# Kernel tuning notes

Hardware: AMD Instinct MI355X
Metric: run time of the kernel (lower is better)

## Reference

```python
import jax, jax.numpy as jnp
import numpy as np
import math

D_MODEL = 2048
HEAD_DIM = 128
NUM_Q_HEADS = 16
NUM_KV_GROUPS = 4


def setup_inputs() -> dict:
    key = jax.random.key(0)
    ks = jax.random.split(key, 9)
    B, S, D = 2, 2048, D_MODEL
    G, HD = NUM_KV_GROUPS, HEAD_DIM
    sd = 1.0 / math.sqrt(D)
    x = jax.random.normal(ks[0], (B, S, D), dtype=jnp.float32)
    # weights stored as [in, out]
    Wq = jax.random.normal(ks[1], (D, D), dtype=jnp.float32) * sd
    bq = jax.random.normal(ks[2], (D,), dtype=jnp.float32) * sd
    Wk = jax.random.normal(ks[3], (D, G * HD), dtype=jnp.float32) * sd
    bk = jax.random.normal(ks[4], (G * HD,), dtype=jnp.float32) * sd
    Wv = jax.random.normal(ks[5], (D, G * HD), dtype=jnp.float32) * sd
    bv = jax.random.normal(ks[6], (G * HD,), dtype=jnp.float32) * sd
    Wo = jax.random.normal(ks[7], (D, D), dtype=jnp.float32) * sd
    bo = jax.random.normal(ks[8], (D,), dtype=jnp.float32) * sd
    return {"x": x, "Wq": Wq, "bq": bq, "Wk": Wk, "bk": bk,
            "Wv": Wv, "bv": bv, "Wo": Wo, "bo": bo}


def reference(x, Wq, bq, Wk, bk, Wv, bv, Wo, bo):
    B, S, D = x.shape
    H, G, HD = NUM_Q_HEADS, NUM_KV_GROUPS, HEAD_DIM
    R = H // G  # q heads per kv group (repeat_interleave factor)
    scale = 1.0 / math.sqrt(HD)
    # projections
    Q = (x @ Wq + bq).reshape(B, S, G, R, HD)   # heads grouped: head h = g*R + r
    K = (x @ Wk + bk).reshape(B, S, G, HD)
    V = (x @ Wv + bv).reshape(B, S, G, HD)
    # scores [B,G,R,S,S]; avoid materializing repeated K/V
    scores = jnp.einsum('bsgrd,btgd->bgrst', Q, K) * scale
    attn = jax.nn.softmax(scores, axis=-1)
    out = jnp.einsum('bgrst,btgd->bsgrd', attn, V)  # [B,S,G,R,HD]
    out = out.reshape(B, S, H * HD)
    return out @ Wo + bo
```

## Files before the change

kernel.cpp:

```cpp
#include <hip/hip_runtime.h>

#define D_MODEL 2048
#define GHD 512
#define HD 128
#define NQH 16
#define B_SZ 2
#define SEQ 2048
#define M_TOT (B_SZ * SEQ)

typedef _Float16 f16;
typedef __fp16 h16x2 __attribute__((ext_vector_type(2)));
typedef _Float16 f16x4 __attribute__((ext_vector_type(4)));
typedef _Float16 f16x8 __attribute__((ext_vector_type(8)));
typedef float f32x4 __attribute__((ext_vector_type(4)));

typedef const __attribute__((address_space(1))) void gvoid;
typedef __attribute__((address_space(3))) void lvoid;
typedef __attribute__((address_space(3))) f16 lf16;

#define BAR() do { asm volatile("" ::: "memory"); \
                   __builtin_amdgcn_s_barrier();  \
                   asm volatile("" ::: "memory"); } while (0)
#define WAIT_VM8() asm volatile("s_waitcnt vmcnt(8)" ::: "memory")
#define WAIT_VM0() asm volatile("s_waitcnt vmcnt(0)" ::: "memory")
#define WAIT_LGKM(N) do { asm volatile("s_waitcnt lgkmcnt(" #N ")" ::: "memory"); \
                          __builtin_amdgcn_sched_barrier(0); } while (0)

template<int OFF>
__device__ __forceinline__ f16x4 tr16(unsigned a) {
    f16x4 d;
    asm volatile("ds_read_b64_tr_b16 %0, %1 offset:%2"
                 : "=v"(d) : "v"(a), "i"(OFF));
    return d;
}

__global__ __launch_bounds__(256) void cast_f16(
    const float* __restrict__ X, f16* __restrict__ Xh)
{
    const size_t i = ((size_t)blockIdx.x * 256 + threadIdx.x) * 8;
    const float4 v0 = *(const float4*)(X + i);
    const float4 v1 = *(const float4*)(X + i + 4);
    f16x8 h;
    h[0] = (f16)v0.x; h[1] = (f16)v0.y; h[2] = (f16)v0.z; h[3] = (f16)v0.w;
    h[4] = (f16)v1.x; h[5] = (f16)v1.y; h[6] = (f16)v1.z; h[7] = (f16)v1.w;
    *(f16x8*)(Xh + i) = h;
}

__global__ __launch_bounds__(256) void transpose_cast(
    const float* __restrict__ W, f16* __restrict__ Th,
    int K, int N, int row_off)
{
    __shared__ float Ls[32][33];
    const int t = threadIdx.x;
    const int n0 = blockIdx.x << 5, k0 = blockIdx.y << 5;
    {
        const int kr = t >> 3, nq = (t & 7) << 2;
        const float4 v = *(const float4*)&W[(size_t)(k0 + kr) * N + n0 + nq];
        Ls[kr][nq + 0] = v.x; Ls[kr][nq + 1] = v.y;
        Ls[kr][nq + 2] = v.z; Ls[kr][nq + 3] = v.w;
    }
    __syncthreads();
    const int nr = t >> 3, kq = (t & 7) << 2;
    f16x4 hv;
#pragma unroll
    for (int e = 0; e < 4; ++e) hv[e] = (f16)Ls[kq + e][nr];
    *(f16x4*)&Th[(size_t)(row_off + n0 + nr) * K + k0 + kq] = hv;
}

template<int BN, bool OUT32>
__global__ __launch_bounds__(256) void gemm_bk64(
    const f16* __restrict__ Agh,
    const f16* __restrict__ BTh,
    const float* __restrict__ bias0, const float* __restrict__ bias1,
    void* __restrict__ C0v, void* __restrict__ C1v,
    int Nsplit, int ld0, int ld1, int K, float outscale)
{
    constexpr int WN = BN / 64;
    constexpr int WM = 4 / WN;
    constexpr int WI = 128 / (WM * 16);
    constexpr int LDK = 72;
    constexpr int NBP = BN / 32;

    __shared__ f16 Ah[128 * LDK];
    __shared__ f16 Bh[BN * LDK];

    const int tid = threadIdx.x;
    const int l = tid & 63, w = tid >> 6;
    const int l15 = l & 15, lq = l >> 4;
    const int wr = w / WN, wc = w % WN;

    const int nwgx = gridDim.x;
    const int orig = blockIdx.y * nwgx + blockIdx.x;
    const int cpx = (nwgx * gridDim.y) >> 3;
    const int sw = (orig & 7) * cpx + (orig >> 3);
    const int m0 = (sw / nwgx) << 7;
    const int n0 = (sw % nwgx) * BN;

    f32x4 acc[WI][4];
#pragma unroll
    for (int i = 0; i < WI; ++i)
#pragma unroll
        for (int j = 0; j < 4; ++j) acc[i][j] = (f32x4){0.f, 0.f, 0.f, 0.f};

    const int srow = tid >> 3;
    const int skc  = (tid & 7) << 3;
    const f16* Ap = Agh + (size_t)(m0 + srow) * K + skc;
    const f16* Bp = BTh + (size_t)(n0 + srow) * K + skc;

    f16x8 av[4], bv[NBP];
#pragma unroll
    for (int p = 0; p < 4; ++p)
        av[p] = *(const f16x8*)(Ap + (size_t)(p * 32) * K);
#pragma unroll
    for (int p = 0; p < NBP; ++p)
        bv[p] = *(const f16x8*)(Bp + (size_t)(p * 32) * K);

    for (int k0 = 0; k0 < K; k0 += 64) {
        __syncthreads();
#pragma unroll
        for (int p = 0; p < 4; ++p)
            *(f16x8*)&Ah[(srow + p * 32) * LDK + skc] = av[p];
#pragma unroll
        for (int p = 0; p < NBP; ++p)
            *(f16x8*)&Bh[(srow + p * 32) * LDK + skc] = bv[p];
        __syncthreads();

        const int kn = k0 + 64;
#pragma unroll
        for (int p = 0; p < 4; ++p)
            av[p] = *(const f16x8*)(Ap + (size_t)(p * 32) * K + kn);
#pragma unroll
        for (int p = 0; p < NBP; ++p)
            bv[p] = *(const f16x8*)(Bp + (size_t)(p * 32) * K + kn);

#pragma unroll
        for (int c = 0; c < 2; ++c) {
            f16x8 afh[WI];
#pragma unroll
            for (int i = 0; i < WI; ++i) {
                const int row = wr * (WI * 16) + i * 16 + l15;
                afh[i] = *(const f16x8*)&Ah[row * LDK + c * 32 + lq * 8];
            }
#pragma unroll
            for (int j = 0; j < 4; ++j) {
                const int bn = wc * 64 + j * 16 + l15;
                const f16x8 bfh = *(const f16x8*)&Bh[bn * LDK + c * 32 + lq * 8];
#pragma unroll
                for (int i = 0; i < WI; ++i)
                    acc[i][j] = __builtin_amdgcn_mfma_f32_16x16x32_f16(afh[i], bfh, acc[i][j], 0, 0, 0);
            }
        }
    }

#pragma unroll
    for (int j = 0; j < 4; ++j) {
        const int ng = n0 + wc * 64 + j * 16 + l15;
        const bool first = ng < Nsplit;
        const float bvf = first ? bias0[ng] : bias1[ng - Nsplit];
        const int nc = first ? ng : ng - Nsplit;
        const int ldc = first ? ld0 : ld1;
#pragma unroll
        for (int i = 0; i < WI; ++i) {
            const int mg = m0 + wr * (WI * 16) + i * 16 + lq * 4;
#pragma unroll
            for (int r = 0; r < 4; ++r) {
                const float v = (acc[i][j][r] + bvf) * outscale;
                if (OUT32)
                    ((float*)(first ? C0v : C1v))[(size_t)(mg + r) * ldc + nc] = v;
                else
                    ((f16*)(first ? C0v : C1v))[(size_t)(mg + r) * ldc + nc] = (f16)v;
            }
        }
    }
}

#define SHUF8(x, y) __builtin_shufflevector(x, y, 0, 1, 2, 3, 4, 5, 6, 7)

__global__ __launch_bounds__(256, 2) void flash_attn_mfma(
    const f16* __restrict__ Q, const f16* __restrict__ Kp,
    const f16* __restrict__ Vp, f16* __restrict__ AOh)
{
    __shared__ f16 KsA[2][64 * 128];
    __shared__ f16 VtA[2][64 * 128];

    const int tid = threadIdx.x;
    const int w = tid >> 6, l = tid & 63;
    const int l15 = l & 15, lq = l >> 4;
    const int b = blockIdx.z, h = blockIdx.y, g = h >> 2;
    const int q0 = blockIdx.x << 7;

    const f16* Qb = Q + (size_t)(b * SEQ + q0) * D_MODEL + h * HD;
    const f16* Kb = Kp + (size_t)b * SEQ * GHD + g * HD;
    const f16* Vb = Vp + (size_t)b * SEQ * GHD + g * HD;

    f16x8 aq[2][4];
#pragma unroll
    for (int rg = 0; rg < 2; ++rg) {
        const f16* qrow = Qb + (size_t)(w * 32 + rg * 16 + l15) * D_MODEL;
#pragma unroll
        for (int c = 0; c < 4; ++c)
            aq[rg][c] = *(const f16x8*)(qrow + c * 32 + lq * 8);
    }

    lf16* Ks3 = (lf16*)&KsA[0][0];
    lf16* Vt3 = (lf16*)&VtA[0][0];
    const f16* ksrc[4]; lf16* kdst[4];
    const f16* vsrc[4]; lf16* vdst[4];
#pragma unroll
    for (int i = 0; i < 4; ++i) {
        const int s = tid + (i << 8);
        {
            const int row = s >> 4, ul = s & 15;
            ksrc[i] = Kb + (size_t)row * GHD + ((ul ^ (row & 7)) << 3);
            kdst[i] = Ks3 + s * 8;
        }
        {
            const int dbit = s & 1, kvlo = (s >> 1) & 3, vlq = (s >> 3) & 3;
            const int jh = (s >> 5) & 1, kc = (s >> 6) & 1, dsub = s >> 7;
            const int kv = (kc << 5) | (jh << 4) | (vlq << 2) | kvlo;
            vsrc[i] = Vb + (size_t)kv * GHD + ((dsub << 4) | (dbit << 3));
            vdst[i] = Vt3 + s * 8;
        }
    }
    const unsigned vta0 = (unsigned)(size_t)(Vt3 + l * 4);
    const unsigned vta1 = vta0 + 16384;

    f32x4 acc_o[2][8];
#pragma unroll
    for (int rg = 0; rg < 2; ++rg)
#pragma unroll
        for (int i = 0; i < 8; ++i) acc_o[rg][i] = (f32x4){0.f, 0.f, 0.f, 0.f};
    float m_q[2] = {-1e30f, -1e30f};
    float l_q[2] = {0.f, 0.f};

    auto issue_tile = [&](int buf, int tile) {
        const size_t koff = (size_t)tile * 64 * GHD;
        const int KO = buf << 13;
#pragma unroll
        for (int i = 0; i < 4; ++i)
            __builtin_amdgcn_global_load_lds((gvoid*)(ksrc[i] + koff),
                                             (lvoid*)(kdst[i] + KO), 16, 0, 0);
#pragma unroll
        for (int i = 0; i < 4; ++i)
            __builtin_amdgcn_global_load_lds((gvoid*)(vsrc[i] + koff),
                                             (lvoid*)(vdst[i] + KO), 16, 0, 0);
    };

    auto compute_tile = [&](const f16* KsB, unsigned vtaB) {
        f32x4 sa[2][4];
        __builtin_amdgcn_s_setprio(1);
#pragma unroll
        for (int cb = 0; cb < 4; ++cb) {
            sa[0][cb] = (f32x4){0.f, 0.f, 0.f, 0.f};
            sa[1][cb] = (f32x4){0.f, 0.f, 0.f, 0.f};
#pragma unroll
            for (int c = 0; c < 4; ++c) {
                const int rk = cb * 16 + l15;
                const f16x8 bk = *(const f16x8*)&KsB[rk * 128 + (((c * 4 + lq) ^ (rk & 7)) << 3)];
                sa[0][cb] = __builtin_amdgcn_mfma_f32_16x16x32_f16(bk, aq[0][c], sa[0][cb], 0, 0, 0);
                sa[1][cb] = __builtin_amdgcn_mfma_f32_16x16x32_f16(bk, aq[1][c], sa[1][cb], 0, 0, 0);
            }
        }
        __builtin_amdgcn_s_setprio(0);

#pragma unroll
        for (int rg = 0; rg < 2; ++rg) {
            float gm = sa[rg][0][0];
#pragma unroll
            for (int cb = 0; cb < 4; ++cb)
#pragma unroll
                for (int reg = 0; reg < 4; ++reg)
                    gm = fmaxf(gm, sa[rg][cb][reg]);
            gm = fmaxf(gm, __shfl_xor(gm, 16));
            gm = fmaxf(gm, __shfl_xor(gm, 32));
            if (__ballot(gm > m_q[rg] + 11.5f)) {
                const float mnew = fmaxf(m_q[rg], gm);
                const float alpha = __builtin_amdgcn_exp2f(m_q[rg] - mnew);
                m_q[rg] = mnew;
                l_q[rg] *= alpha;
                f32x4 av;
#pragma unroll
                for (int reg = 0; reg < 4; ++reg)
                    av[reg] = __shfl(alpha, lq * 4 + reg);
#pragma unroll
                for (int db = 0; db < 8; ++db) acc_o[rg][db] *= av;
            }
        }

        f16x4 va0 = tr16<0>(vtaB),    vb0 = tr16<512>(vtaB);
        f16x4 va1 = tr16<1024>(vtaB), vb1 = tr16<1536>(vtaB);
        f16x4 ca0 = tr16<2048>(vtaB), cb0 = tr16<2560>(vtaB);
        f16x4 ca1 = tr16<3072>(vtaB), cb1 = tr16<3584>(vtaB);

        f16x8 pa[2][2];
#pragma unroll
        for (int rg = 0; rg < 2; ++rg) {
            float ps = 0.f;
#pragma unroll
            for (int cb = 0; cb < 4; ++cb)
#pragma unroll
                for (int reg = 0; reg < 4; ++reg) {
                    const float p = __builtin_amdgcn_exp2f(sa[rg][cb][reg] - m_q[rg]);
                    sa[rg][cb][reg] = p;
                    ps += p;
                }
            l_q[rg] += ps;
#pragma unroll
            for (int kc = 0; kc < 2; ++kc) {
                union { h16x2 h2[4]; f16x8 h8; } u;
                u.h2[0] = __builtin_amdgcn_cvt_pkrtz(sa[rg][2 * kc][0], sa[rg][2 * kc][1]);
                u.h2[1] = __builtin_amdgcn_cvt_pkrtz(sa[rg][2 * kc][2], sa[rg][2 * kc][3]);
                u.h2[2] = __builtin_amdgcn_cvt_pkrtz(sa[rg][2 * kc + 1][0], sa[rg][2 * kc + 1][1]);
                u.h2[3] = __builtin_amdgcn_cvt_pkrtz(sa[rg][2 * kc + 1][2], sa[rg][2 * kc + 1][3]);
                pa[rg][kc] = u.h8;
            }
        }

        WAIT_LGKM(4);
        f16x8 v0 = SHUF8(va0, vb0), v1 = SHUF8(va1, vb1);
#pragma unroll
        for (int db = 0; db < 8; ++db) {
            f16x4 ma0, mb0, ma1, mb1;
            if (db < 6) {
                switch (db) {
                case 0: ma0=tr16<4096>(vtaB);  mb0=tr16<4608>(vtaB);  ma1=tr16<5120>(vtaB);  mb1=tr16<5632>(vtaB);  break;
                case 1: ma0=tr16<6144>(vtaB);  mb0=tr16<6656>(vtaB);  ma1=tr16<7168>(vtaB);  mb1=tr16<7680>(vtaB);  break;
                case 2: ma0=tr16<8192>(vtaB);  mb0=tr16<8704>(vtaB);  ma1=tr16<9216>(vtaB);  mb1=tr16<9728>(vtaB);  break;
                case 3: ma0=tr16<10240>(vtaB); mb0=tr16<10752>(vtaB); ma1=tr16<11264>(vtaB); mb1=tr16<11776>(vtaB); break;
                case 4: ma0=tr16<12288>(vtaB); mb0=tr16<12800>(vtaB); ma1=tr16<13312>(vtaB); mb1=tr16<13824>(vtaB); break;
                default:ma0=tr16<14336>(vtaB); mb0=tr16<14848>(vtaB); ma1=tr16<15360>(vtaB); mb1=tr16<15872>(vtaB); break;
                }
                WAIT_LGKM(4);
            } else if (db == 6) {
                WAIT_LGKM(0);
            }
            f16x8 n0, n1;
            if (db < 7) { n0 = SHUF8(ca0, cb0); n1 = SHUF8(ca1, cb1); }
            __builtin_amdgcn_s_setprio(1);
            acc_o[0][db] = __builtin_amdgcn_mfma_f32_16x16x32_f16(pa[0][0], v0, acc_o[0][db], 0, 0, 0);
            acc_o[1][db] = __builtin_amdgcn_mfma_f32_16x16x32_f16(pa[1][0], v0, acc_o[1][db], 0, 0, 0);
            acc_o[0][db] = __builtin_amdgcn_mfma_f32_16x16x32_f16(pa[0][1], v1, acc_o[0][db], 0, 0, 0);
            acc_o[1][db] = __builtin_amdgcn_mfma_f32_16x16x32_f16(pa[1][1], v1, acc_o[1][db], 0, 0, 0);
            __builtin_amdgcn_s_setprio(0);
            if (db < 7) {
                v0 = n0; v1 = n1;
                ca0 = ma0; cb0 = mb0; ca1 = ma1; cb1 = mb1;
            }
        }
    };

    issue_tile(0, 0);
#pragma unroll 1
    for (int t2 = 0; t2 < 16; ++t2) {
        const int kt0 = t2 << 1;
        issue_tile(1, kt0 + 1);
        WAIT_VM8();
        BAR();
        compute_tile(&KsA[0][0], vta0);
        BAR();
        if (t2 < 15) {
            issue_tile(0, kt0 + 2);
            WAIT_VM8();
        } else {
            WAIT_VM0();
        }
        BAR();
        compute_tile(&KsA[1][0], vta1);
        BAR();
    }

    const size_t obase = (size_t)(b * SEQ + q0 + w * 32) * D_MODEL + h * HD;
#pragma unroll
    for (int rg = 0; rg < 2; ++rg) {
        float lr = l_q[rg];
        lr += __shfl_xor(lr, 16);
        lr += __shfl_xor(lr, 32);
        float inv_l[4];
#pragma unroll
        for (int reg = 0; reg < 4; ++reg)
            inv_l[reg] = 1.f / __shfl(lr, lq * 4 + reg);
#pragma unroll
        for (int db = 0; db < 8; ++db) {
#pragma unroll
            for (int reg = 0; reg < 4; ++reg) {
                const size_t off = obase + (size_t)(rg * 16 + lq * 4 + reg) * D_MODEL + db * 16 + l15;
                AOh[off] = (f16)(acc_o[rg][db][reg] * inv_l[reg]);
            }
        }
    }
}

extern "C" void kernel_launch(void* const* d_in, const int* in_sizes, int n_in,
                              void* d_out, int out_size, void* d_ws, size_t ws_size,
                              hipStream_t stream)
{
    const float* x  = (const float*)d_in[0];
    const float* Wq = (const float*)d_in[1];
    const float* bq = (const float*)d_in[2];
    const float* Wk = (const float*)d_in[3];
    const float* bk = (const float*)d_in[4];
    const float* Wv = (const float*)d_in[5];
    const float* bv = (const float*)d_in[6];
    const float* Wo = (const float*)d_in[7];
    const float* bo = (const float*)d_in[8];
    float* out = (float*)d_out;

    f16* base  = (f16*)d_ws;
    f16* xh    = base;
    f16* WkvT  = base + 16777216;
    f16* WqoT  = base + 20971520;
    f16* Qp    = base + 29360128;
    f16* Kp    = base + 37748736;
    f16* Vp    = base + 39845888;
    f16* AOh   = xh;

    const dim3 blk(256);
    const float qscale = 0.08838834764831845f * 1.4426950408889634f;

    cast_f16<<<dim3(M_TOT * D_MODEL / 8 / 256), blk, 0, stream>>>(x, xh);
    transpose_cast<<<dim3(64, 64), blk, 0, stream>>>(Wq, WqoT, 2048, 2048, 0);
    transpose_cast<<<dim3(16, 64), blk, 0, stream>>>(Wk, WkvT, 2048, 512, 0);
    transpose_cast<<<dim3(16, 64), blk, 0, stream>>>(Wv, WkvT, 2048, 512, 512);

    gemm_bk64<128, false><<<dim3(16, 32), blk, 0, stream>>>(
        xh, WqoT, bq, bq, Qp, Qp, 2048, 2048, 2048, 2048, qscale);
    gemm_bk64<64, false><<<dim3(16, 32), blk, 0, stream>>>(
        xh, WkvT, bk, bv, Kp, Vp, 512, 512, 512, 2048, 1.0f);

    transpose_cast<<<dim3(64, 64), blk, 0, stream>>>(Wo, WqoT, 2048, 2048, 0);

    flash_attn_mfma<<<dim3(SEQ / 128, NQH, B_SZ), blk, 0, stream>>>(Qp, Kp, Vp, AOh);

    gemm_bk64<128, true><<<dim3(16, 32), blk, 0, stream>>>(
        AOh, WqoT, bo, bo, out, out, 2048, 2048, 2048, 2048, 1.0f);
}
```

Measured before the change: 227.4 us.

## Fuse Q/K/V projections into one GEMM and use BK=128 for output projection

Concatenates transposed Wq, Wk and Wv into one weight buffer and runs a single GEMM with a 24x32 grid that routes each column block to Q, K or V with the matching bias and scale. This removes a kernel launch and the low-occupancy separate KV GEMM. The GEMM is also templated on BK, and the output projection now uses BK=128, which halves its K-loop iterations at the cost of more shared memory and registers per block. The workspace layout is compacted to match.

Result: slower. 238.4 us (+4.9%).

```diff
diff --git a/kernel.cpp b/kernel.cpp
--- a/kernel.cpp
+++ b/kernel.cpp
@@ -67,19 +67,24 @@
     *(f16x4*)&Th[(size_t)(row_off + n0 + nr) * K + k0 + kq] = hv;
 }
 
-template<int BN, bool OUT32>
-__global__ __launch_bounds__(256) void gemm_bk64(
-    const f16* __restrict__ Agh,
-    const f16* __restrict__ BTh,
-    const float* __restrict__ bias0, const float* __restrict__ bias1,
-    void* __restrict__ C0v, void* __restrict__ C1v,
-    int Nsplit, int ld0, int ld1, int K, float outscale)
+template<int BN, int BK, bool QKV>
+__global__ __launch_bounds__(256) void gemm_f16(
+    const f16* __restrict__ Agh, const f16* __restrict__ BTh,
+    const float* __restrict__ b0, const float* __restrict__ b1,
+    const float* __restrict__ b2,
+    f16* __restrict__ Qo, f16* __restrict__ Ko, f16* __restrict__ Vo,
+    float* __restrict__ Fo,
+    int K, float qscale)
 {
     constexpr int WN = BN / 64;
     constexpr int WM = 4 / WN;
     constexpr int WI = 128 / (WM * 16);
-    constexpr int LDK = 72;
-    constexpr int NBP = BN / 32;
+    constexpr int LDK = BK + 8;
+    constexpr int CH  = BK / 8;
+    constexpr int RPP = 256 / CH;
+    constexpr int AP  = 128 / RPP;
+    constexpr int BP  = BN / RPP;
+    constexpr int NC  = BK / 32;
 
     __shared__ f16 Ah[128 * LDK];
     __shared__ f16 Bh[BN * LDK];
@@ -102,39 +107,39 @@
 #pragma unroll
         for (int j = 0; j < 4; ++j) acc[i][j] = (f32x4){0.f, 0.f, 0.f, 0.f};
 
-    const int srow = tid >> 3;
-    const int skc  = (tid & 7) << 3;
+    const int srow = tid / CH;
+    const int skc  = (tid % CH) * 8;
     const f16* Ap = Agh + (size_t)(m0 + srow) * K + skc;
     const f16* Bp = BTh + (size_t)(n0 + srow) * K + skc;
 
-    f16x8 av[4], bv[NBP];
-#pragma unroll
-    for (int p = 0; p < 4; ++p)
-        av[p] = *(const f16x8*)(Ap + (size_t)(p * 32) * K);
-#pragma unroll
-    for (int p = 0; p < NBP; ++p)
-        bv[p] = *(const f16x8*)(Bp + (size_t)(p * 32) * K);
-
-    for (int k0 = 0; k0 < K; k0 += 64) {
+    f16x8 av[AP], bvv[BP];
+#pragma unroll
+    for (int p = 0; p < AP; ++p)
+        av[p] = *(const f16x8*)(Ap + (size_t)(p * RPP) * K);
+#pragma unroll
+    for (int p = 0; p < BP; ++p)
+        bvv[p] = *(const f16x8*)(Bp + (size_t)(p * RPP) * K);
+
+    for (int k0 = 0; k0 < K; k0 += BK) {
         __syncthreads();
 #pragma unroll
-        for (int p = 0; p < 4; ++p)
-            *(f16x8*)&Ah[(srow + p * 32) * LDK + skc] = av[p];
-#pragma unroll
-        for (int p = 0; p < NBP; ++p)
-            *(f16x8*)&Bh[(srow + p * 32) * LDK + skc] = bv[p];
+        for (int p = 0; p < AP; ++p)
+            *(f16x8*)&Ah[(srow + p * RPP) * LDK + skc] = av[p];
+#pragma unroll
+        for (int p = 0; p < BP; ++p)
+            *(f16x8*)&Bh[(srow + p * RPP) * LDK + skc] = bvv[p];
         __syncthreads();
 
-        const int kn = k0 + 64;
-#pragma unroll
-        for (int p = 0; p < 4; ++p)
-            av[p] = *(const f16x8*)(Ap + (size_t)(p * 32) * K + kn);
-#pragma unroll
-        for (int p = 0; p < NBP; ++p)
-            bv[p] = *(const f16x8*)(Bp + (size_t)(p * 32) * K + kn);
-
-#pragma unroll
-        for (int c = 0; c < 2; ++c) {
+        const int kn = k0 + BK;
+#pragma unroll
+        for (int p = 0; p < AP; ++p)
+            av[p] = *(const f16x8*)(Ap + (size_t)(p * RPP) * K + kn);
+#pragma unroll
+        for (int p = 0; p < BP; ++p)
+            bvv[p] = *(const f16x8*)(Bp + (size_t)(p * RPP) * K + kn);
+
+#pragma unroll
+        for (int c = 0; c < NC; ++c) {
             f16x8 afh[WI];
 #pragma unroll
             for (int i = 0; i < WI; ++i) {
@@ -155,20 +160,26 @@
 #pragma unroll
     for (int j = 0; j < 4; ++j) {
         const int ng = n0 + wc * 64 + j * 16 + l15;
-        const bool first = ng < Nsplit;
-        const float bvf = first ? bias0[ng] : bias1[ng - Nsplit];
-        const int nc = first ? ng : ng - Nsplit;
-        const int ldc = first ? ld0 : ld1;
+        float bias, osc = 1.f;
+        f16* outp = nullptr;
+        int nc = ng, ldc = 2048;
+        if constexpr (QKV) {
+            if (ng < 2048)      { bias = b0[ng];        outp = Qo; osc = qscale; }
+            else if (ng < 2560) { bias = b1[ng - 2048]; outp = Ko; nc = ng - 2048; ldc = 512; }
+            else                { bias = b2[ng - 2560]; outp = Vo; nc = ng - 2560; ldc = 512; }
+        } else {
+            bias = b0[ng];
+        }
 #pragma unroll
         for (int i = 0; i < WI; ++i) {
             const int mg = m0 + wr * (WI * 16) + i * 16 + lq * 4;
 #pragma unroll
             for (int r = 0; r < 4; ++r) {
-                const float v = (acc[i][j][r] + bvf) * outscale;
-                if (OUT32)
-                    ((float*)(first ? C0v : C1v))[(size_t)(mg + r) * ldc + nc] = v;
+                const float v = (acc[i][j][r] + bias) * osc;
+                if constexpr (QKV)
+                    outp[(size_t)(mg + r) * ldc + nc] = (f16)v;
                 else
-                    ((f16*)(first ? C0v : C1v))[(size_t)(mg + r) * ldc + nc] = (f16)v;
+                    Fo[(size_t)(mg + r) * 2048 + nc] = v;
             }
         }
     }
@@ -405,32 +416,29 @@
     const float* bo = (const float*)d_in[8];
     float* out = (float*)d_out;
 
-    f16* base  = (f16*)d_ws;
-    f16* xh    = base;
-    f16* WkvT  = base + 16777216;
-    f16* WqoT  = base + 20971520;
-    f16* Qp    = base + 29360128;
-    f16* Kp    = base + 37748736;
-    f16* Vp    = base + 39845888;
-    f16* AOh   = xh;
+    f16* base   = (f16*)d_ws;
+    f16* xh     = base;
+    f16* WqkvT  = base + 8388608;
+    f16* Qp     = base + 14680064;
+    f16* Kp     = base + 23068672;
+    f16* Vp     = base + 25165824;
+    f16* AOh    = xh;
 
     const dim3 blk(256);
     const float qscale = 0.08838834764831845f * 1.4426950408889634f;
 
     cast_f16<<<dim3(M_TOT * D_MODEL / 8 / 256), blk, 0, stream>>>(x, xh);
-    transpose_cast<<<dim3(64, 64), blk, 0, stream>>>(Wq, WqoT, 2048, 2048, 0);
-    transpose_cast<<<dim3(16, 64), blk, 0, stream>>>(Wk, WkvT, 2048, 512, 0);
-    transpose_cast<<<dim3(16, 64), blk, 0, stream>>>(Wv, WkvT, 2048, 512, 512);
-
-    gemm_bk64<128, false><<<dim3(16, 32), blk, 0, stream>>>(
-        xh, WqoT, bq, bq, Qp, Qp, 2048, 2048, 2048, 2048, qscale);
-    gemm_bk64<64, false><<<dim3(16, 32), blk, 0, stream>>>(
-        xh, WkvT, bk, bv, Kp, Vp, 512, 512, 512, 2048, 1.0f);
-
-    transpose_cast<<<dim3(64, 64), blk, 0, stream>>>(Wo, WqoT, 2048, 2048, 0);
+    transpose_cast<<<dim3(64, 64), blk, 0, stream>>>(Wq, WqkvT, 2048, 2048, 0);
+    transpose_cast<<<dim3(16, 64), blk, 0, stream>>>(Wk, WqkvT, 2048, 512, 2048);
+    transpose_cast<<<dim3(16, 64), blk, 0, stream>>>(Wv, WqkvT, 2048, 512, 2560);
+
+    gemm_f16<128, 64, true><<<dim3(24, 32), blk, 0, stream>>>(
+        xh, WqkvT, bq, bk, bv, Qp, Kp, Vp, nullptr, 2048, qscale);
+
+    transpose_cast<<<dim3(64, 64), blk, 0, stream>>>(Wo, WqkvT, 2048, 2048, 0);
 
     flash_attn_mfma<<<dim3(SEQ / 128, NQH, B_SZ), blk, 0, stream>>>(Qp, Kp, Vp, AOh);
 
-    gemm_bk64<128, true><<<dim3(16, 32), blk, 0, stream>>>(
-        AOh, WqoT, bo, bo, out, out, 2048, 2048, 2048, 2048, 1.0f);
-}
+    gemm_f16<128, 128, false><<<dim3(16, 32), blk, 0, stream>>>(
+        AOh, WqkvT, bo, bo, bo, nullptr, nullptr, nullptr, out, 2048, 1.0f);
+}
```
